# Performance work log

Measured on AMD Instinct MI355X. Metric: run time of the kernel, lower is better.

The kernel has to match this reference:

```python
import math
import jax, jax.numpy as jnp
import numpy as np

B, A, U, S, E, HYP, H = 16384, 32, 64, 2048, 32, 64, 4
ATTEND_REG_COEF = 1e-3


def setup_inputs() -> dict:
    key = jax.random.key(0)
    ks = jax.random.split(key, 12)
    sc = 0.05
    return {
        "agent_qs": jax.random.normal(ks[0], (B, A), jnp.float32),
        "states": jax.random.normal(ks[1], (B, S), jnp.float32),
        # per-head selector hypernet: Linear(S,HYP)+ReLU+Linear(HYP,E,no bias)
        "sel_w1": jax.random.normal(ks[2], (H, S, HYP), jnp.float32) * sc,
        "sel_b1": jax.random.normal(ks[3], (H, HYP), jnp.float32) * sc,
        "sel_w2": jax.random.normal(ks[4], (H, HYP, E), jnp.float32) * sc,
        # per-head key extractor: Linear(U,E,no bias)
        "key_w": jax.random.normal(ks[5], (H, U, E), jnp.float32) * sc,
        # V net: Linear(S,E)+ReLU+Linear(E,1)
        "v_w1": jax.random.normal(ks[6], (S, E), jnp.float32) * sc,
        "v_b1": jax.random.normal(ks[7], (E,), jnp.float32) * sc,
        "v_w2": jax.random.normal(ks[8], (E, 1), jnp.float32) * sc,
        "v_b2": jax.random.normal(ks[9], (1,), jnp.float32) * sc,
    }


def reference(agent_qs, states, sel_w1, sel_b1, sel_w2, key_w, v_w1, v_b1, v_w2, v_b2):
    # nonlinear=False, weighted_head=False, state_bias=True (defaults used here)
    unit_states = states[:, : A * U].reshape(-1, A, U)  # [B, A, U]

    # per-head selectors: [B, H, E]
    h1 = jax.nn.relu(jnp.einsum("bs,hsk->bhk", states, sel_w1) + sel_b1[None])
    selectors = jnp.einsum("bhk,hke->bhe", h1, sel_w2)

    # per-head, per-agent keys: [B, H, A, E]
    keys = jnp.einsum("bau,hue->bhae", unit_states, key_w)

    # attention logits [B, H, A] (matches selector @ stacked-keys in torch)
    logits = jnp.einsum("bhe,bhae->bha", selectors, keys)
    weights = jax.nn.softmax(logits / math.sqrt(E), axis=-1)  # [B, H, A]

    head_attend = jnp.sum(weights, axis=1)  # [B, A]

    v = jax.nn.relu(states @ v_w1 + v_b1) @ v_w2 + v_b2  # [B, 1]

    # coef * sum over heads of mean(logits_h ** 2)
    attend_mag_regs = ATTEND_REG_COEF * jnp.sum(jnp.mean(logits ** 2, axis=(0, 2)))

    # per-head entropy: -(p * log(p + 1e-8)).sum(agents).mean(batch) -> [H]
    head_entropies = -jnp.mean(
        jnp.sum(weights * jnp.log(weights + 1e-8), axis=-1), axis=0
    )

    return head_attend, v, attend_mag_regs, head_entropies
```

## Files before the change

### kernel.cpp

```cpp
#include <hip/hip_runtime.h>
#include <hip/hip_bf16.h>

#define B_N 16384
#define A_N 32
#define U_N 64
#define S_N 2048
#define E_N 32
#define HYP_N 64
#define H_N 4
#define NREAL 288
#define NPADG 320

#define H1_STRIDE 312
#define TS_STRIDE 260

#define WS_WT    0
#define WS_MB    1310720
#define WS_PMAG  (WS_MB + 32768)
#define WS_PENT  (WS_PMAG + 65536)
#define WS_H1    (WS_PENT + 262144)

#define OUT_V   (B_N * A_N)
#define OUT_MAG (OUT_V + B_N)
#define OUT_ENT (OUT_MAG + 1)

typedef __attribute__((ext_vector_type(8))) short bf16x8_t;
typedef __attribute__((ext_vector_type(4))) float floatx4_t;

#define AS1(p) ((const __attribute__((address_space(1))) void*)(p))
#define AS3(p) ((__attribute__((address_space(3))) void*)(p))

__device__ __forceinline__ unsigned short f2b(float f) {
    union { float f; unsigned u; } v; v.f = f;
    unsigned r = v.u + 0x7FFFu + ((v.u >> 16) & 1u);
    return (unsigned short)(r >> 16);
}

__global__ __launch_bounds__(256) void pack_w_kernel(
        const float* __restrict__ sel_w1, const float* __restrict__ v_w1,
        const float* __restrict__ sel_w2, const float* __restrict__ key_w,
        unsigned short* __restrict__ Wt, unsigned short* __restrict__ Mb) {
    int idx = blockIdx.x * 256 + threadIdx.x;
    if (idx < NPADG * S_N) {
        int n = idx >> 11;
        int k = idx & 2047;
        float val = 0.0f;
        if (n < 256) {
            int h = n >> 6, kk = n & 63;
            val = sel_w1[((size_t)h * S_N + k) * HYP_N + kk];
        } else if (n < NREAL) {
            val = v_w1[(size_t)k * E_N + (n - 256)];
        }
        Wt[idx] = f2b(val);
    } else if (idx < NPADG * S_N + H_N * U_N * HYP_N) {
        int j = idx - NPADG * S_N;
        int h = j >> 12, u = (j >> 6) & 63, k = j & 63;
        const float* kw = key_w + ((size_t)h * U_N + u) * E_N;
        const float* w2 = sel_w2 + ((size_t)h * HYP_N + k) * E_N;
        float s = 0.0f;
#pragma unroll
        for (int e = 0; e < E_N; ++e) s = fmaf(kw[e], w2[e], s);
        Mb[j] = f2b(s);
    }
}

#define FM_BM 32
#define FM_BK 64
#define NIT   (S_N / FM_BK)

__global__ __launch_bounds__(512, 6) void gemm_h1_kernel(
        const float* __restrict__ states, const unsigned short* __restrict__ Wt,
        const float* __restrict__ sel_b1, const float* __restrict__ v_b1,
        unsigned short* __restrict__ h1g) {
    __shared__ __align__(16) char pool[4096 + 40960];
    unsigned short* Asm = (unsigned short*)pool;
    unsigned short* Bsm = (unsigned short*)(pool + 4096);

    const int t = threadIdx.x;
    const int lane = t & 63;
    const int w = t >> 6;
    const int m0 = blockIdx.x * FM_BM;
    const int miw = (w & 1) * 16;
    const int nw = (w >> 1) * 80;

    const int ar = t >> 3, acl = t & 7;
    const float* ap = states + (size_t)(m0 + ar) * S_N + acl * 8;

    floatx4_t acc[5] = {};
    float4 a0, a1;

    if (t < 256) {
        a0 = *(const float4*)(ap);
        a1 = *(const float4*)(ap + 4);
        int ph = acl ^ (ar & 7);
        uint4 o;
        o.x = (unsigned)f2b(a0.x) | ((unsigned)f2b(a0.y) << 16);
        o.y = (unsigned)f2b(a0.z) | ((unsigned)f2b(a0.w) << 16);
        o.z = (unsigned)f2b(a1.x) | ((unsigned)f2b(a1.y) << 16);
        o.w = (unsigned)f2b(a1.z) | ((unsigned)f2b(a1.w) << 16);
        *(uint4*)(Asm + (size_t)(ar * 8 + ph) * 8) = o;
    }
#pragma unroll
    for (int i = 0; i < 5; ++i) {
        int p = i * 512 + t, n = p >> 3, sl = p & 7;
        int cl = sl ^ (n & 7);
        __builtin_amdgcn_global_load_lds(AS1(Wt + (size_t)n * S_N + cl * 8),
                                         AS3(Bsm + p * 8), 16, 0, 0);
    }
    if (t < 256) {
        a0 = *(const float4*)(ap + FM_BK);
        a1 = *(const float4*)(ap + FM_BK + 4);
    }
    __syncthreads();

    for (int it = 0; it < NIT; ++it) {
#pragma unroll
        for (int s = 0; s < 2; ++s) {
            const int c = s * 4 + (lane >> 4);
            int r = miw + (lane & 15);
            int pha = c ^ (r & 7);
            bf16x8_t afr = *(const bf16x8_t*)(Asm + r * 64 + pha * 8);
#pragma unroll
            for (int nt = 0; nt < 5; ++nt) {
                int n = nw + nt * 16 + (lane & 15);
                int ph = c ^ (n & 7);
                bf16x8_t bfr = *(const bf16x8_t*)(Bsm + n * 64 + ph * 8);
                acc[nt] = __builtin_amdgcn_mfma_f32_16x16x32_bf16(
                    afr, bfr, acc[nt], 0, 0, 0);
            }
        }
        __syncthreads();
        if (it < NIT - 1) {
            int k0 = (it + 1) * FM_BK;
            if (t < 256) {
                int ph = acl ^ (ar & 7);
                uint4 o;
                o.x = (unsigned)f2b(a0.x) | ((unsigned)f2b(a0.y) << 16);
                o.y = (unsigned)f2b(a0.z) | ((unsigned)f2b(a0.w) << 16);
                o.z = (unsigned)f2b(a1.x) | ((unsigned)f2b(a1.y) << 16);
                o.w = (unsigned)f2b(a1.z) | ((unsigned)f2b(a1.w) << 16);
                *(uint4*)(Asm + (size_t)(ar * 8 + ph) * 8) = o;
            }
#pragma unroll
            for (int i = 0; i < 5; ++i) {
                int p = i * 512 + t, n = p >> 3, sl = p & 7;
                int cl = sl ^ (n & 7);
                __builtin_amdgcn_global_load_lds(
                    AS1(Wt + (size_t)n * S_N + k0 + cl * 8),
                    AS3(Bsm + p * 8), 16, 0, 0);
            }
            if (it < NIT - 2 && t < 256) {
                const float* g = ap + (it + 2) * FM_BK;
                a0 = *(const float4*)(g);
                a1 = *(const float4*)(g + 4);
            }
            __syncthreads();
        }
    }

    unsigned short* hrow = h1g + (size_t)m0 * H1_STRIDE;
#pragma unroll
    for (int nt = 0; nt < 5; ++nt) {
        int n = nw + nt * 16 + (lane & 15);
        if (n >= NREAL) continue;
        float bias = (n < 256) ? sel_b1[n] : v_b1[n - 256];
        int slot = (n < 256) ? ((n >> 6) * 72 + (n & 63))
                             : (((n - 256) >> 3) * 72 + 64 + ((n - 256) & 7));
#pragma unroll
        for (int rg = 0; rg < 4; ++rg) {
            int r = miw + (lane >> 4) * 4 + rg;
            float v = acc[nt][rg] + bias;
            hrow[(size_t)r * H1_STRIDE + slot] = f2b(v > 0.0f ? v : 0.0f);
        }
    }
}

#define K2_BM 16

__global__ __launch_bounds__(256, 8) void attend_kernel(
        const float* __restrict__ states, const unsigned short* __restrict__ h1g,
        const unsigned short* __restrict__ Mb,
        const float* __restrict__ v_w2, const float* __restrict__ v_b2,
        float* __restrict__ out, float* __restrict__ pmag, float* __restrict__ pent) {
    __shared__ __align__(16) float tsb[K2_BM * TS_STRIDE];
    const int t = threadIdx.x;
    const int lane = t & 63;
    const int w = t >> 6;
    const int m0 = blockIdx.x * K2_BM;

    {
        const int h = w;
        const unsigned short* hbase =
            h1g + (size_t)(m0 + (lane & 15)) * H1_STRIDE + h * 72;
        floatx4_t tacc[4] = {};
#pragma unroll
        for (int s = 0; s < 2; ++s) {
            int k0 = s * 32 + (lane >> 4) * 8;
            bf16x8_t afr = *(const bf16x8_t*)(hbase + k0);
#pragma unroll
            for (int ut = 0; ut < 4; ++ut) {
                int u = ut * 16 + (lane & 15);
                bf16x8_t bfr = *(const bf16x8_t*)(Mb + ((size_t)(h * U_N + u) * 64) + k0);
                tacc[ut] = __builtin_amdgcn_mfma_f32_16x16x32_bf16(
                    afr, bfr, tacc[ut], 0, 0, 0);
            }
        }
#pragma unroll
        for (int ut = 0; ut < 4; ++ut)
#pragma unroll
            for (int rg = 0; rg < 4; ++rg) {
                int r = (lane >> 4) * 4 + rg;
                int u = ut * 16 + (lane & 15);
                tsb[r * TS_STRIDE + h * U_N + u] = tacc[ut][rg];
            }
    }
    __syncthreads();

    const int a = lane & 31, uh = lane >> 5;
    for (int rr = 0; rr < 4; ++rr) {
        const int r = w * 4 + rr;
        const int b = m0 + r;
        const float* up = states + (size_t)b * S_N + a * 64 + uh * 32;
        const float* tp = &tsb[r * TS_STRIDE + uh * 32];
        float pl[4] = {0.0f, 0.0f, 0.0f, 0.0f};
        float4 c0 = ((const float4*)up)[0];
        float4 c1 = ((const float4*)up)[1];
#pragma unroll
        for (int i = 0; i < 8; ++i) {
            float4 s4 = c0;
            c0 = c1;
            if (i < 6) c1 = ((const float4*)up)[i + 2];
#pragma unroll
            for (int h = 0; h < 4; ++h) {
                float4 t4 = *(const float4*)(tp + h * U_N + i * 4);
                pl[h] = fmaf(s4.x, t4.x, pl[h]);
                pl[h] = fmaf(s4.y, t4.y, pl[h]);
                pl[h] = fmaf(s4.z, t4.z, pl[h]);
                pl[h] = fmaf(s4.w, t4.w, pl[h]);
            }
        }
#pragma unroll
        for (int h = 0; h < 4; ++h)
            pl[h] += __shfl_xor(pl[h], 32, 64);

        float mg = pl[0]*pl[0] + pl[1]*pl[1] + pl[2]*pl[2] + pl[3]*pl[3];
#pragma unroll
        for (int o = 16; o > 0; o >>= 1) mg += __shfl_xor(mg, o, 32);

        float hatt = 0.0f;
        float entv[4];
#pragma unroll
        for (int h = 0; h < 4; ++h) {
            float x = pl[h] * 0.17677669529663687f;
            float p = __expf(x);
            float den = p, px = p * x;
#pragma unroll
            for (int o = 16; o > 0; o >>= 1) {
                den += __shfl_xor(den, o, 32);
                px  += __shfl_xor(px,  o, 32);
            }
            float inv = 1.0f / den;
            hatt = fmaf(p, inv, hatt);
            entv[h] = px * inv - __logf(den);
        }

        if (uh == 0) {
            out[(size_t)b * A_N + a] = hatt;
            unsigned hv = h1g[(size_t)b * H1_STRIDE + (a >> 3) * 72 + 64 + (a & 7)];
            union { unsigned u; float f; } cv; cv.u = hv << 16;
            float pv = cv.f * v_w2[a];
#pragma unroll
            for (int o = 16; o > 0; o >>= 1) pv += __shfl_xor(pv, o, 32);
            if (a == 0) {
                out[OUT_V + b] = pv + v_b2[0];
                pmag[b] = mg;
#pragma unroll
                for (int h = 0; h < 4; ++h) pent[(size_t)h * B_N + b] = entv[h];
            }
        }
    }
}

__global__ __launch_bounds__(256) void finalize_kernel(
        const float* __restrict__ pmag, const float* __restrict__ pent,
        float* __restrict__ out) {
    int which = blockIdx.x;
    const float* src = (which == 0) ? pmag : (pent + (size_t)(which - 1) * B_N);
    float s = 0.0f;
    for (int i = threadIdx.x; i < B_N; i += 256) s += src[i];
#pragma unroll
    for (int o = 32; o > 0; o >>= 1) s += __shfl_xor(s, o, 64);
    __shared__ float red[4];
    if ((threadIdx.x & 63) == 0) red[threadIdx.x >> 6] = s;
    __syncthreads();
    if (threadIdx.x == 0) {
        float tot = red[0] + red[1] + red[2] + red[3];
        if (which == 0) out[OUT_MAG] = 1e-3f * tot / (float)(B_N * A_N);
        else out[OUT_ENT + which - 1] = -tot / (float)B_N;
    }
}

extern "C" void kernel_launch(void* const* d_in, const int* in_sizes, int n_in,
                              void* d_out, int out_size, void* d_ws, size_t ws_size,
                              hipStream_t stream) {
    const float* states = (const float*)d_in[1];
    const float* sel_w1 = (const float*)d_in[2];
    const float* sel_b1 = (const float*)d_in[3];
    const float* sel_w2 = (const float*)d_in[4];
    const float* key_w  = (const float*)d_in[5];
    const float* v_w1   = (const float*)d_in[6];
    const float* v_b1   = (const float*)d_in[7];
    const float* v_w2   = (const float*)d_in[8];
    const float* v_b2   = (const float*)d_in[9];
    float* out = (float*)d_out;
    char* wsb  = (char*)d_ws;

    unsigned short* Wt  = (unsigned short*)(wsb + WS_WT);
    unsigned short* Mb  = (unsigned short*)(wsb + WS_MB);
    float* pmag         = (float*)(wsb + WS_PMAG);
    float* pent         = (float*)(wsb + WS_PENT);
    unsigned short* h1g = (unsigned short*)(wsb + WS_H1);

    pack_w_kernel<<<dim3((NPADG * S_N + H_N * U_N * HYP_N + 255) / 256),
                    dim3(256), 0, stream>>>(sel_w1, v_w1, sel_w2, key_w, Wt, Mb);
    gemm_h1_kernel<<<dim3(B_N / FM_BM), dim3(512), 0, stream>>>(
        states, Wt, sel_b1, v_b1, h1g);
    attend_kernel<<<dim3(B_N / K2_BM), dim3(256), 0, stream>>>(
        states, h1g, Mb, v_w2, v_b2, out, pmag, pent);
    finalize_kernel<<<dim3(5), dim3(256), 0, stream>>>(pmag, pent, out);
}
```

Baseline: 283.2 us.

## Fuse selector-key projection into GEMM epilogue and double-buffer the main GEMM

The main GEMM now tiles 64 rows per block and double-buffers its LDS tiles, so it needs one barrier per K step instead of two. It keeps the ReLU'd hidden layer in shared memory and runs the small h1×M MFMA projection in its epilogue. That projection result goes to global memory as fp32, and the v-net hidden activations go out separately as bf16. The attention kernel no longer does the MFMA step and reads the precomputed projections from global memory. This trades the bf16 h1 round trip for a larger fp32 intermediate (16 MB written and read back), and the bigger tile lowers occupancy (launch bounds 512,2).

New measurement: 301.5 us. +6.4%, slower.

```diff
diff --git a/kernel.cpp b/kernel.cpp
--- a/kernel.cpp
+++ b/kernel.cpp
@@ -11,14 +11,14 @@
 #define NREAL 288
 #define NPADG 320
 
-#define H1_STRIDE 312
-#define TS_STRIDE 260
+#define H1B_STRIDE 264
 
 #define WS_WT    0
 #define WS_MB    1310720
 #define WS_PMAG  (WS_MB + 32768)
 #define WS_PENT  (WS_PMAG + 65536)
-#define WS_H1    (WS_PENT + 262144)
+#define WS_T     (WS_PENT + 262144)
+#define WS_HV    (WS_T + 16777216)
 
 #define OUT_V   (B_N * A_N)
 #define OUT_MAG (OUT_V + B_N)
@@ -34,6 +34,17 @@
     union { float f; unsigned u; } v; v.f = f;
     unsigned r = v.u + 0x7FFFu + ((v.u >> 16) & 1u);
     return (unsigned short)(r >> 16);
+}
+__device__ __forceinline__ float b2f(unsigned x) {
+    union { unsigned u; float f; } v; v.u = x << 16; return v.f;
+}
+__device__ __forceinline__ uint4 pack_bf16x8(float4 a0, float4 a1) {
+    uint4 o;
+    o.x = (unsigned)f2b(a0.x) | ((unsigned)f2b(a0.y) << 16);
+    o.y = (unsigned)f2b(a0.z) | ((unsigned)f2b(a0.w) << 16);
+    o.z = (unsigned)f2b(a1.x) | ((unsigned)f2b(a1.y) << 16);
+    o.w = (unsigned)f2b(a1.z) | ((unsigned)f2b(a1.w) << 16);
+    return o;
 }
 
 __global__ __launch_bounds__(256) void pack_w_kernel(
@@ -64,42 +75,39 @@
     }
 }
 
-#define FM_BM 32
+#define FM_BM 64
 #define FM_BK 64
 #define NIT   (S_N / FM_BK)
-
-__global__ __launch_bounds__(512, 6) void gemm_h1_kernel(
+#define ASM_SH (FM_BM * FM_BK)
+#define BSM_SH (NPADG * FM_BK)
+
+__global__ __launch_bounds__(512, 2) void gemm_t_kernel(
         const float* __restrict__ states, const unsigned short* __restrict__ Wt,
         const float* __restrict__ sel_b1, const float* __restrict__ v_b1,
-        unsigned short* __restrict__ h1g) {
-    __shared__ __align__(16) char pool[4096 + 40960];
+        const unsigned short* __restrict__ Mb,
+        float* __restrict__ tg, unsigned short* __restrict__ hv) {
+    __shared__ __align__(16) char pool[2 * ASM_SH * 2 + 2 * BSM_SH * 2];
     unsigned short* Asm = (unsigned short*)pool;
-    unsigned short* Bsm = (unsigned short*)(pool + 4096);
+    unsigned short* Bsm = (unsigned short*)(pool + 2 * ASM_SH * 2);
+    unsigned short* h1b = (unsigned short*)pool;
 
     const int t = threadIdx.x;
     const int lane = t & 63;
     const int w = t >> 6;
     const int m0 = blockIdx.x * FM_BM;
-    const int miw = (w & 1) * 16;
+    const int miw = (w & 1) * 32;
     const int nw = (w >> 1) * 80;
 
     const int ar = t >> 3, acl = t & 7;
     const float* ap = states + (size_t)(m0 + ar) * S_N + acl * 8;
-
-    floatx4_t acc[5] = {};
+    const int aph = acl ^ (ar & 7);
+
+    floatx4_t acc[2][5] = {};
     float4 a0, a1;
 
-    if (t < 256) {
-        a0 = *(const float4*)(ap);
-        a1 = *(const float4*)(ap + 4);
-        int ph = acl ^ (ar & 7);
-        uint4 o;
-        o.x = (unsigned)f2b(a0.x) | ((unsigned)f2b(a0.y) << 16);
-        o.y = (unsigned)f2b(a0.z) | ((unsigned)f2b(a0.w) << 16);
-        o.z = (unsigned)f2b(a1.x) | ((unsigned)f2b(a1.y) << 16);
-        o.w = (unsigned)f2b(a1.z) | ((unsigned)f2b(a1.w) << 16);
-        *(uint4*)(Asm + (size_t)(ar * 8 + ph) * 8) = o;
-    }
+    a0 = *(const float4*)(ap);
+    a1 = *(const float4*)(ap + 4);
+    *(uint4*)(Asm + (size_t)(ar * 8 + aph) * 8) = pack_bf16x8(a0, a1);
 #pragma unroll
     for (int i = 0; i < 5; ++i) {
         int p = i * 512 + t, n = p >> 3, sl = p & 7;
@@ -107,121 +115,136 @@
         __builtin_amdgcn_global_load_lds(AS1(Wt + (size_t)n * S_N + cl * 8),
                                          AS3(Bsm + p * 8), 16, 0, 0);
     }
-    if (t < 256) {
-        a0 = *(const float4*)(ap + FM_BK);
-        a1 = *(const float4*)(ap + FM_BK + 4);
-    }
+    a0 = *(const float4*)(ap + FM_BK);
+    a1 = *(const float4*)(ap + FM_BK + 4);
     __syncthreads();
 
+    int cur = 0;
     for (int it = 0; it < NIT; ++it) {
-#pragma unroll
-        for (int s = 0; s < 2; ++s) {
-            const int c = s * 4 + (lane >> 4);
-            int r = miw + (lane & 15);
-            int pha = c ^ (r & 7);
-            bf16x8_t afr = *(const bf16x8_t*)(Asm + r * 64 + pha * 8);
-#pragma unroll
-            for (int nt = 0; nt < 5; ++nt) {
-                int n = nw + nt * 16 + (lane & 15);
-                int ph = c ^ (n & 7);
-                bf16x8_t bfr = *(const bf16x8_t*)(Bsm + n * 64 + ph * 8);
-                acc[nt] = __builtin_amdgcn_mfma_f32_16x16x32_bf16(
-                    afr, bfr, acc[nt], 0, 0, 0);
-            }
-        }
-        __syncthreads();
         if (it < NIT - 1) {
+            unsigned short* An = Asm + (cur ^ 1) * ASM_SH;
+            unsigned short* Bn = Bsm + (cur ^ 1) * BSM_SH;
             int k0 = (it + 1) * FM_BK;
-            if (t < 256) {
-                int ph = acl ^ (ar & 7);
-                uint4 o;
-                o.x = (unsigned)f2b(a0.x) | ((unsigned)f2b(a0.y) << 16);
-                o.y = (unsigned)f2b(a0.z) | ((unsigned)f2b(a0.w) << 16);
-                o.z = (unsigned)f2b(a1.x) | ((unsigned)f2b(a1.y) << 16);
-                o.w = (unsigned)f2b(a1.z) | ((unsigned)f2b(a1.w) << 16);
-                *(uint4*)(Asm + (size_t)(ar * 8 + ph) * 8) = o;
-            }
+            *(uint4*)(An + (size_t)(ar * 8 + aph) * 8) = pack_bf16x8(a0, a1);
 #pragma unroll
             for (int i = 0; i < 5; ++i) {
                 int p = i * 512 + t, n = p >> 3, sl = p & 7;
                 int cl = sl ^ (n & 7);
                 __builtin_amdgcn_global_load_lds(
                     AS1(Wt + (size_t)n * S_N + k0 + cl * 8),
-                    AS3(Bsm + p * 8), 16, 0, 0);
-            }
-            if (it < NIT - 2 && t < 256) {
+                    AS3(Bn + p * 8), 16, 0, 0);
+            }
+            if (it < NIT - 2) {
                 const float* g = ap + (it + 2) * FM_BK;
                 a0 = *(const float4*)(g);
                 a1 = *(const float4*)(g + 4);
             }
-            __syncthreads();
-        }
-    }
-
-    unsigned short* hrow = h1g + (size_t)m0 * H1_STRIDE;
+        }
+        const unsigned short* Ac = Asm + cur * ASM_SH;
+        const unsigned short* Bc = Bsm + cur * BSM_SH;
+#pragma unroll
+        for (int s = 0; s < 2; ++s) {
+            const int c = s * 4 + (lane >> 4);
+            bf16x8_t afr[2];
+#pragma unroll
+            for (int mt = 0; mt < 2; ++mt) {
+                int r = miw + mt * 16 + (lane & 15);
+                afr[mt] = *(const bf16x8_t*)(Ac + r * 64 + (c ^ (r & 7)) * 8);
+            }
+#pragma unroll
+            for (int nt = 0; nt < 5; ++nt) {
+                int n = nw + nt * 16 + (lane & 15);
+                bf16x8_t bfr = *(const bf16x8_t*)(Bc + n * 64 + (c ^ (n & 7)) * 8);
+                acc[0][nt] = __builtin_amdgcn_mfma_f32_16x16x32_bf16(
+                    afr[0], bfr, acc[0][nt], 0, 0, 0);
+                acc[1][nt] = __builtin_amdgcn_mfma_f32_16x16x32_bf16(
+                    afr[1], bfr, acc[1][nt], 0, 0, 0);
+            }
+        }
+        __syncthreads();
+        cur ^= 1;
+    }
+
 #pragma unroll
     for (int nt = 0; nt < 5; ++nt) {
         int n = nw + nt * 16 + (lane & 15);
-        if (n >= NREAL) continue;
-        float bias = (n < 256) ? sel_b1[n] : v_b1[n - 256];
-        int slot = (n < 256) ? ((n >> 6) * 72 + (n & 63))
-                             : (((n - 256) >> 3) * 72 + 64 + ((n - 256) & 7));
-#pragma unroll
-        for (int rg = 0; rg < 4; ++rg) {
-            int r = miw + (lane >> 4) * 4 + rg;
-            float v = acc[nt][rg] + bias;
-            hrow[(size_t)r * H1_STRIDE + slot] = f2b(v > 0.0f ? v : 0.0f);
-        }
-    }
-}
-
-#define K2_BM 16
-
-__global__ __launch_bounds__(256, 8) void attend_kernel(
-        const float* __restrict__ states, const unsigned short* __restrict__ h1g,
-        const unsigned short* __restrict__ Mb,
+        if (n < 256) {
+            float bias = sel_b1[n];
+#pragma unroll
+            for (int mt = 0; mt < 2; ++mt)
+#pragma unroll
+                for (int rg = 0; rg < 4; ++rg) {
+                    int r = miw + mt * 16 + (lane >> 4) * 4 + rg;
+                    float v = acc[mt][nt][rg] + bias;
+                    h1b[r * H1B_STRIDE + n] = f2b(v > 0.0f ? v : 0.0f);
+                }
+        } else if (n < NREAL) {
+            int j = n - 256;
+            float bias = v_b1[j];
+#pragma unroll
+            for (int mt = 0; mt < 2; ++mt)
+#pragma unroll
+                for (int rg = 0; rg < 4; ++rg) {
+                    int r = miw + mt * 16 + (lane >> 4) * 4 + rg;
+                    float v = acc[mt][nt][rg] + bias;
+                    hv[(size_t)(m0 + r) * 32 + j] = f2b(v > 0.0f ? v : 0.0f);
+                }
+        }
+    }
+    __syncthreads();
+
+    {
+        const int h = w >> 1;
+        const int rb = (w & 1) * 32;
+        floatx4_t tacc[2][4] = {};
+#pragma unroll
+        for (int s = 0; s < 2; ++s) {
+            int k0 = s * 32 + (lane >> 4) * 8;
+            bf16x8_t afr[2];
+#pragma unroll
+            for (int mt = 0; mt < 2; ++mt)
+                afr[mt] = *(const bf16x8_t*)(
+                    h1b + (rb + mt * 16 + (lane & 15)) * H1B_STRIDE + h * 64 + k0);
+#pragma unroll
+            for (int ut = 0; ut < 4; ++ut) {
+                int u = ut * 16 + (lane & 15);
+                bf16x8_t bfr = *(const bf16x8_t*)(Mb + ((size_t)(h * U_N + u) * 64) + k0);
+#pragma unroll
+                for (int mt = 0; mt < 2; ++mt)
+                    tacc[mt][ut] = __builtin_amdgcn_mfma_f32_16x16x32_bf16(
+                        afr[mt], bfr, tacc[mt][ut], 0, 0, 0);
+            }
+        }
+#pragma unroll
+        for (int mt = 0; mt < 2; ++mt)
+#pragma unroll
+            for (int ut = 0; ut < 4; ++ut)
+#pragma unroll
+                for (int rg = 0; rg < 4; ++rg) {
+                    int b = m0 + rb + mt * 16 + (lane >> 4) * 4 + rg;
+                    int u = ut * 16 + (lane & 15);
+                    tg[((size_t)b * H_N + h) * U_N + u] = tacc[mt][ut][rg];
+                }
+    }
+}
+
+#define L_BM 16
+
+__global__ __launch_bounds__(256, 8) void attend_l_kernel(
+        const float* __restrict__ states, const float* __restrict__ tg,
+        const unsigned short* __restrict__ hv,
         const float* __restrict__ v_w2, const float* __restrict__ v_b2,
         float* __restrict__ out, float* __restrict__ pmag, float* __restrict__ pent) {
-    __shared__ __align__(16) float tsb[K2_BM * TS_STRIDE];
     const int t = threadIdx.x;
     const int lane = t & 63;
     const int w = t >> 6;
-    const int m0 = blockIdx.x * K2_BM;
-
-    {
-        const int h = w;
-        const unsigned short* hbase =
-            h1g + (size_t)(m0 + (lane & 15)) * H1_STRIDE + h * 72;
-        floatx4_t tacc[4] = {};
-#pragma unroll
-        for (int s = 0; s < 2; ++s) {
-            int k0 = s * 32 + (lane >> 4) * 8;
-            bf16x8_t afr = *(const bf16x8_t*)(hbase + k0);
-#pragma unroll
-            for (int ut = 0; ut < 4; ++ut) {
-                int u = ut * 16 + (lane & 15);
-                bf16x8_t bfr = *(const bf16x8_t*)(Mb + ((size_t)(h * U_N + u) * 64) + k0);
-                tacc[ut] = __builtin_amdgcn_mfma_f32_16x16x32_bf16(
-                    afr, bfr, tacc[ut], 0, 0, 0);
-            }
-        }
-#pragma unroll
-        for (int ut = 0; ut < 4; ++ut)
-#pragma unroll
-            for (int rg = 0; rg < 4; ++rg) {
-                int r = (lane >> 4) * 4 + rg;
-                int u = ut * 16 + (lane & 15);
-                tsb[r * TS_STRIDE + h * U_N + u] = tacc[ut][rg];
-            }
-    }
-    __syncthreads();
-
+    const int m0 = blockIdx.x * L_BM;
     const int a = lane & 31, uh = lane >> 5;
+
     for (int rr = 0; rr < 4; ++rr) {
-        const int r = w * 4 + rr;
-        const int b = m0 + r;
+        const int b = m0 + w * 4 + rr;
         const float* up = states + (size_t)b * S_N + a * 64 + uh * 32;
-        const float* tp = &tsb[r * TS_STRIDE + uh * 32];
+        const float* tp = tg + (size_t)b * (H_N * U_N) + uh * 32;
         float pl[4] = {0.0f, 0.0f, 0.0f, 0.0f};
         float4 c0 = ((const float4*)up)[0];
         float4 c1 = ((const float4*)up)[1];
@@ -266,9 +289,7 @@
 
         if (uh == 0) {
             out[(size_t)b * A_N + a] = hatt;
-            unsigned hv = h1g[(size_t)b * H1_STRIDE + (a >> 3) * 72 + 64 + (a & 7)];
-            union { unsigned u; float f; } cv; cv.u = hv << 16;
-            float pv = cv.f * v_w2[a];
+            float pv = b2f((unsigned)hv[(size_t)b * 32 + a]) * v_w2[a];
 #pragma unroll
             for (int o = 16; o > 0; o >>= 1) pv += __shfl_xor(pv, o, 32);
             if (a == 0) {
@@ -319,13 +340,14 @@
     unsigned short* Mb  = (unsigned short*)(wsb + WS_MB);
     float* pmag         = (float*)(wsb + WS_PMAG);
     float* pent         = (float*)(wsb + WS_PENT);
-    unsigned short* h1g = (unsigned short*)(wsb + WS_H1);
+    float* tg           = (float*)(wsb + WS_T);
+    unsigned short* hv  = (unsigned short*)(wsb + WS_HV);
 
     pack_w_kernel<<<dim3((NPADG * S_N + H_N * U_N * HYP_N + 255) / 256),
                     dim3(256), 0, stream>>>(sel_w1, v_w1, sel_w2, key_w, Wt, Mb);
-    gemm_h1_kernel<<<dim3(B_N / FM_BM), dim3(512), 0, stream>>>(
-        states, Wt, sel_b1, v_b1, h1g);
-    attend_kernel<<<dim3(B_N / K2_BM), dim3(256), 0, stream>>>(
-        states, h1g, Mb, v_w2, v_b2, out, pmag, pent);
+    gemm_t_kernel<<<dim3(B_N / FM_BM), dim3(512), 0, stream>>>(
+        states, Wt, sel_b1, v_b1, Mb, tg, hv);
+    attend_l_kernel<<<dim3(B_N / L_BM), dim3(256), 0, stream>>>(
+        states, tg, hv, v_w2, v_b2, out, pmag, pent);
     finalize_kernel<<<dim3(5), dim3(256), 0, stream>>>(pmag, pent, out);
 }
```

## Fuse hypernet GEMM and attention kernels, keeping h1 in shared memory

Applied to the files above, without the earlier changes.

Merges the h1 GEMM kernel and the attention kernel into a single launch. The bf16 h1 tile is kept in LDS instead of being written to and re-read from a global workspace, and the B-tile buffer is reused for the per-row projection scratch. This removes one launch and the global round trip for h1. In exchange, LDS use per block grows and the occupancy hint drops from 6 to 4 blocks, and the attention stage now runs with 8 waves over 32 rows per block.

After: 277.4 us. 2.1% less time.

```diff
diff --git a/kernel.cpp b/kernel.cpp
--- a/kernel.cpp
+++ b/kernel.cpp
@@ -11,14 +11,10 @@
 #define NREAL 288
 #define NPADG 320
 
-#define H1_STRIDE 312
-#define TS_STRIDE 260
-
 #define WS_WT    0
 #define WS_MB    1310720
 #define WS_PMAG  (WS_MB + 32768)
 #define WS_PENT  (WS_PMAG + 65536)
-#define WS_H1    (WS_PENT + 262144)
 
 #define OUT_V   (B_N * A_N)
 #define OUT_MAG (OUT_V + B_N)
@@ -34,6 +30,9 @@
     union { float f; unsigned u; } v; v.f = f;
     unsigned r = v.u + 0x7FFFu + ((v.u >> 16) & 1u);
     return (unsigned short)(r >> 16);
+}
+__device__ __forceinline__ float b2f(unsigned x) {
+    union { unsigned u; float f; } v; v.u = x << 16; return v.f;
 }
 
 __global__ __launch_bounds__(256) void pack_w_kernel(
@@ -67,14 +66,20 @@
 #define FM_BM 32
 #define FM_BK 64
 #define NIT   (S_N / FM_BK)
-
-__global__ __launch_bounds__(512, 6) void gemm_h1_kernel(
+#define H1_STRIDE 312
+#define TS_STRIDE 260
+
+__global__ __launch_bounds__(512, 4) void fused_kernel(
         const float* __restrict__ states, const unsigned short* __restrict__ Wt,
         const float* __restrict__ sel_b1, const float* __restrict__ v_b1,
-        unsigned short* __restrict__ h1g) {
-    __shared__ __align__(16) char pool[4096 + 40960];
+        const unsigned short* __restrict__ Mb,
+        const float* __restrict__ v_w2, const float* __restrict__ v_b2,
+        float* __restrict__ out, float* __restrict__ pmag, float* __restrict__ pent) {
+    __shared__ __align__(16) char pool[4096 + 40960 + H1_STRIDE * FM_BM * 2];
     unsigned short* Asm = (unsigned short*)pool;
     unsigned short* Bsm = (unsigned short*)(pool + 4096);
+    float*          tsb = (float*)(pool + 4096);
+    unsigned short* h1b = (unsigned short*)(pool + 4096 + 40960);
 
     const int t = threadIdx.x;
     const int lane = t & 63;
@@ -158,7 +163,6 @@
         }
     }
 
-    unsigned short* hrow = h1g + (size_t)m0 * H1_STRIDE;
 #pragma unroll
     for (int nt = 0; nt < 5; ++nt) {
         int n = nw + nt * 16 + (lane & 15);
@@ -170,33 +174,20 @@
         for (int rg = 0; rg < 4; ++rg) {
             int r = miw + (lane >> 4) * 4 + rg;
             float v = acc[nt][rg] + bias;
-            hrow[(size_t)r * H1_STRIDE + slot] = f2b(v > 0.0f ? v : 0.0f);
-        }
-    }
-}
-
-#define K2_BM 16
-
-__global__ __launch_bounds__(256, 8) void attend_kernel(
-        const float* __restrict__ states, const unsigned short* __restrict__ h1g,
-        const unsigned short* __restrict__ Mb,
-        const float* __restrict__ v_w2, const float* __restrict__ v_b2,
-        float* __restrict__ out, float* __restrict__ pmag, float* __restrict__ pent) {
-    __shared__ __align__(16) float tsb[K2_BM * TS_STRIDE];
-    const int t = threadIdx.x;
-    const int lane = t & 63;
-    const int w = t >> 6;
-    const int m0 = blockIdx.x * K2_BM;
+            h1b[r * H1_STRIDE + slot] = f2b(v > 0.0f ? v : 0.0f);
+        }
+    }
+    __syncthreads();
 
     {
-        const int h = w;
-        const unsigned short* hbase =
-            h1g + (size_t)(m0 + (lane & 15)) * H1_STRIDE + h * 72;
+        const int h = w >> 1;
+        const int rb = (w & 1) * 16;
         floatx4_t tacc[4] = {};
 #pragma unroll
         for (int s = 0; s < 2; ++s) {
             int k0 = s * 32 + (lane >> 4) * 8;
-            bf16x8_t afr = *(const bf16x8_t*)(hbase + k0);
+            bf16x8_t afr = *(const bf16x8_t*)(h1b + (rb + (lane & 15)) * H1_STRIDE
+                                              + h * 72 + k0);
 #pragma unroll
             for (int ut = 0; ut < 4; ++ut) {
                 int u = ut * 16 + (lane & 15);
@@ -209,7 +200,7 @@
         for (int ut = 0; ut < 4; ++ut)
 #pragma unroll
             for (int rg = 0; rg < 4; ++rg) {
-                int r = (lane >> 4) * 4 + rg;
+                int r = rb + (lane >> 4) * 4 + rg;
                 int u = ut * 16 + (lane & 15);
                 tsb[r * TS_STRIDE + h * U_N + u] = tacc[ut][rg];
             }
@@ -266,9 +257,8 @@
 
         if (uh == 0) {
             out[(size_t)b * A_N + a] = hatt;
-            unsigned hv = h1g[(size_t)b * H1_STRIDE + (a >> 3) * 72 + 64 + (a & 7)];
-            union { unsigned u; float f; } cv; cv.u = hv << 16;
-            float pv = cv.f * v_w2[a];
+            float pv = b2f((unsigned)h1b[r * H1_STRIDE + (a >> 3) * 72 + 64 + (a & 7)])
+                       * v_w2[a];
 #pragma unroll
             for (int o = 16; o > 0; o >>= 1) pv += __shfl_xor(pv, o, 32);
             if (a == 0) {
@@ -319,13 +309,10 @@
     unsigned short* Mb  = (unsigned short*)(wsb + WS_MB);
     float* pmag         = (float*)(wsb + WS_PMAG);
     float* pent         = (float*)(wsb + WS_PENT);
-    unsigned short* h1g = (unsigned short*)(wsb + WS_H1);
 
     pack_w_kernel<<<dim3((NPADG * S_N + H_N * U_N * HYP_N + 255) / 256),
                     dim3(256), 0, stream>>>(sel_w1, v_w1, sel_w2, key_w, Wt, Mb);
-    gemm_h1_kernel<<<dim3(B_N / FM_BM), dim3(512), 0, stream>>>(
-        states, Wt, sel_b1, v_b1, h1g);
-    attend_kernel<<<dim3(B_N / K2_BM), dim3(256), 0, stream>>>(
-        states, h1g, Mb, v_w2, v_b2, out, pmag, pent);
+    fused_kernel<<<dim3(B_N / FM_BM), dim3(512), 0, stream>>>(
+        states, Wt, sel_b1, v_b1, Mb, v_w2, v_b2, out, pmag, pent);
     finalize_kernel<<<dim3(5), dim3(256), 0, stream>>>(pmag, pent, out);
 }
```
